# Optimization experiments

Measured on AMD Instinct MI355X. Metric: run time of the kernel, lower is better.

## Reference

```python
import jax, jax.numpy as jnp
import numpy as np
from jax import lax

B, L, P, CIN, N, HD, PH, K = 2048, 96, 96, 8, 64, 64, 8, 3
DIM_C = CIN * N  # 512


def _silu(x):
    return x * jax.nn.sigmoid(x)


def _lin(x, w, b):
    return x @ w.T + b


def setup_inputs() -> dict:
    key = jax.random.key(0)
    ks = iter(jax.random.split(key, 64))

    def w(shape):
        fan_in = shape[-1]
        return (jax.random.normal(next(ks), shape, jnp.float32) / np.sqrt(fan_in)).astype(jnp.float32)

    inp = {"x": jax.random.normal(next(ks), (B, L, CIN), jnp.float32)}
    # x_proj: 5 Linears (enc_in->h, h->h, h->h, h->h, h->N), SiLU between (dropout=eval/identity)
    inp["xp_w0"] = w((HD, CIN)); inp["xp_b0"] = jnp.zeros((HD,), jnp.float32)
    inp["xp_w1"] = w((HD, HD));  inp["xp_b1"] = jnp.zeros((HD,), jnp.float32)
    inp["xp_w2"] = w((HD, HD));  inp["xp_b2"] = jnp.zeros((HD,), jnp.float32)
    inp["xp_w3"] = w((HD, HD));  inp["xp_b3"] = jnp.zeros((HD,), jnp.float32)
    inp["xp_w4"] = w((N, HD));   inp["xp_b4"] = jnp.zeros((N,), jnp.float32)
    # x_proj_: Linear(N,h), SiLU, Linear(h,N)
    inp["xpp_w0"] = w((HD, N)); inp["xpp_b0"] = jnp.zeros((HD,), jnp.float32)
    inp["xpp_w1"] = w((N, HD)); inp["xpp_b1"] = jnp.zeros((N,), jnp.float32)
    # depthwise dilated Conv1d: weight (N, 1, K)
    inp["conv_w"] = w((N, 1, K)); inp["conv_b"] = jnp.zeros((N,), jnp.float32)
    inp["span_A"] = jnp.asarray(0.1, jnp.float32)
    # compress: Linear(N*L, PH)
    inp["comp_w"] = w((PH, N * L)); inp["comp_b"] = jnp.zeros((PH,), jnp.float32)
    # a_ode.net: Linear(PH,h), SiLU, Linear(h,PH), Tanh
    inp["net_w0"] = w((HD, PH)); inp["net_b0"] = jnp.zeros((HD,), jnp.float32)
    inp["net_w1"] = w((PH, HD)); inp["net_b1"] = jnp.zeros((PH,), jnp.float32)
    # lat2out: Linear(PH,8), SiLU, Linear(8,N)
    inp["lo_w0"] = w((8, PH)); inp["lo_b0"] = jnp.zeros((8,), jnp.float32)
    inp["lo_w1"] = w((N, 8));  inp["lo_b1"] = jnp.zeros((N,), jnp.float32)
    # lat2out_c: Linear(PH,8), SiLU, Linear(8, CIN*N)
    inp["lc_w0"] = w((8, PH));     inp["lc_b0"] = jnp.zeros((8,), jnp.float32)
    inp["lc_w1"] = w((DIM_C, 8));  inp["lc_b1"] = jnp.zeros((DIM_C,), jnp.float32)
    # lat2out_z: Linear(N,N), SiLU, Linear(N, CIN)
    inp["lz_w0"] = w((N, N));   inp["lz_b0"] = jnp.zeros((N,), jnp.float32)
    inp["lz_w1"] = w((CIN, N)); inp["lz_b1"] = jnp.zeros((CIN,), jnp.float32)
    return inp


def reference(x, xp_w0, xp_b0, xp_w1, xp_b1, xp_w2, xp_b2, xp_w3, xp_b3, xp_w4, xp_b4,
              xpp_w0, xpp_b0, xpp_w1, xpp_b1, conv_w, conv_b, span_A, comp_w, comp_b,
              net_w0, net_b0, net_w1, net_b1, lo_w0, lo_b0, lo_w1, lo_b1,
              lc_w0, lc_b0, lc_w1, lc_b1, lz_w0, lz_b0, lz_w1, lz_b1):
    Bsz = x.shape[0]

    def x_proj(t):
        h = _silu(_lin(t, xp_w0, xp_b0))
        h = _silu(_lin(h, xp_w1, xp_b1))
        h = _silu(_lin(h, xp_w2, xp_b2))
        h = _silu(_lin(h, xp_w3, xp_b3))
        return _lin(h, xp_w4, xp_b4)

    x_old = x_proj(x[:, :L])                       # (B, L, N)
    hist = x_old.transpose(0, 2, 1)                # (B, N, L)
    pad = (K - 1) * 2                              # 4
    conv = lax.conv_general_dilated(
        hist, conv_w, window_strides=(1,), padding=[(pad, pad)],
        rhs_dilation=(2,), dimension_numbers=("NCH", "OIH", "NCH"),
        feature_group_count=N) + conv_b[None, :, None]
    hist = _silu(conv)[:, :, -L:]                  # (B, N, L)
    hist_f = hist.transpose(0, 2, 1).reshape(Bsz, L * N)
    vector_F = _lin(hist_f, comp_w, comp_b)        # (B, PH)

    a0 = vector_F
    z0 = x_proj(x[:, L - 1])                       # (B, N)

    # Householder matrix H = I - 2 v v^T with v = normalize(x_proj_(z0))
    v = _lin(_silu(_lin(z0, xpp_w0, xpp_b0)), xpp_w1, xpp_b1)
    v = v / (jnp.linalg.norm(v, axis=-1, keepdims=True) + 1e-8)
    Hh = jnp.eye(N, dtype=x.dtype)[None] - 2.0 * v[:, :, None] * v[:, None, :]  # (B,N,N)

    dt = jnp.clip(span_A, 1e-8, 7.0)               # uniform Euler step size
    s0 = jnp.concatenate([a0, z0], axis=-1)        # (B, PH+N)

    def step(s, _):
        a = s[:, :PH]
        z = s[:, PH:]
        da = jnp.tanh(_lin(_silu(_lin(a, net_w0, net_b0)), net_w1, net_b1))  # (B,PH)
        d = _lin(_silu(_lin(a, lo_w0, lo_b0)), lo_w1, lo_b1)                 # (B,N)
        # dz = H^T diag(d) H z   (fused; avoids materializing A_mat)
        Hz = jnp.einsum('bjk,bk->bj', Hh, z)
        dz = jnp.einsum('bj,bji->bi', d * Hz, Hh)
        s_new = s + dt * jnp.concatenate([da, dz], axis=-1)
        return s_new, s_new

    _, sol = lax.scan(step, s0, None, length=P)    # (P, B, PH+N) == sol[1:]

    c_traj = sol[:, :, :PH]                        # (P, B, PH)
    z_traj = sol[:, :, PH:]                        # (P, B, N)

    C = _lin(_silu(_lin(c_traj, lc_w0, lc_b0)), lc_w1, lc_b1)  # (P, B, CIN*N)
    C = C.reshape(P, Bsz, CIN, N)
    y_hat_c = jnp.einsum('pbcn,pbn->pbc', C, z_traj)           # (P, B, CIN)
    added_z = _lin(_silu(_lin(z_traj, lz_w0, lz_b0)), lz_w1, lz_b1)
    x_pred = (y_hat_c + added_z).transpose(1, 0, 2)            # (B, P, CIN)

    x_rec = x[:, :L, :]
    return (x_rec, x_pred)
```

## Files before the change

### kernel.cpp

```cpp
#include <hip/hip_runtime.h>
#include <cstdint>
#include <cstddef>

#define BB 2048
#define LL 96
#define PP 96
#define NN 64
#define HSTRIDE 68

typedef __attribute__((ext_vector_type(8))) short short8;
typedef __attribute__((ext_vector_type(4))) float f32x4;

union U4S8 { uint4 u; short8 s; };

__device__ __forceinline__ float siluf(float x) {
  return x * __builtin_amdgcn_rcpf(1.0f + __expf(-x));
}
__device__ __forceinline__ float tanhf_fast(float x) {
  return 1.0f - 2.0f * __builtin_amdgcn_rcpf(1.0f + __expf(2.0f * x));
}
__device__ __forceinline__ float rlane(float x, int l) {
  return __int_as_float(__builtin_amdgcn_readlane(__float_as_int(x), l));
}

template <int CTRL>
__device__ __forceinline__ float dppadd(float x) {
  int y = __builtin_amdgcn_update_dpp(0, __float_as_int(x), CTRL, 0xF, 0xF, false);
  return x + __int_as_float(y);
}
template <int CTRL>
__device__ __forceinline__ float dppmov(float x) {
  int y = __builtin_amdgcn_update_dpp(0, __float_as_int(x), CTRL, 0xF, 0xF, false);
  return __int_as_float(y);
}

__device__ __forceinline__ float addswap16(float x) {
#if __has_builtin(__builtin_amdgcn_permlane16_swap)
  auto r = __builtin_amdgcn_permlane16_swap(__float_as_uint(x), __float_as_uint(x), false, false);
  return __uint_as_float(r[0]) + __uint_as_float(r[1]);
#else
  return x + __shfl_xor(x, 16, 64);
#endif
}
__device__ __forceinline__ float addswap32(float x) {
#if __has_builtin(__builtin_amdgcn_permlane32_swap)
  auto r = __builtin_amdgcn_permlane32_swap(__float_as_uint(x), __float_as_uint(x), false, false);
  return __uint_as_float(r[0]) + __uint_as_float(r[1]);
#else
  return x + __shfl_xor(x, 32, 64);
#endif
}
__device__ __forceinline__ float movswap32(float x, bool hi) {
#if __has_builtin(__builtin_amdgcn_permlane32_swap)
  auto r = __builtin_amdgcn_permlane32_swap(__float_as_uint(x), __float_as_uint(x), false, false);
  return __uint_as_float(hi ? r[0] : r[1]);
#else
  return __shfl_xor(x, 32, 64);
#endif
}

__device__ __forceinline__ float wave_sum(float x) {
  x = dppadd<0xB1>(x);
  x = dppadd<0x4E>(x);
  x = dppadd<0x141>(x);
  x = dppadd<0x128>(x);
  x = addswap16(x);
  x = addswap32(x);
  return x;
}

__device__ __forceinline__ uint32_t packpair(float f) {
  uint32_t b = __float_as_uint(f);
  uint32_t h = b & 0xFFFF0000u;
  float r = f - __uint_as_float(h);
  return (h >> 16) | (__float_as_uint(r) & 0xFFFF0000u);
}
__device__ __forceinline__ uint32_t rot16(uint32_t x) {
#if __has_builtin(__builtin_amdgcn_alignbit)
  return __builtin_amdgcn_alignbit(x, x, 16);
#else
  return (x >> 16) | (x << 16);
#endif
}
__device__ __forceinline__ uint4 rot16x4(uint4 u) {
  return make_uint4(rot16(u.x), rot16(u.y), rot16(u.z), rot16(u.w));
}
__device__ __forceinline__ short8 as8(uint4 u) { U4S8 c; c.u = u; return c.s; }

__global__ __launch_bounds__(256, 2) void k_xproj(
    const float* __restrict__ x,
    const float* __restrict__ w0, const float* __restrict__ b0,
    const float* __restrict__ w1, const float* __restrict__ b1,
    const float* __restrict__ w2, const float* __restrict__ b2,
    const float* __restrict__ w3, const float* __restrict__ b3,
    const float* __restrict__ w4, const float* __restrict__ b4,
    float* __restrict__ x_old, float* __restrict__ out)
{
  __shared__ uint32_t hbuf[128 * HSTRIDE];
  __shared__ uint32_t wbufA[64 * HSTRIDE];
  __shared__ uint32_t wbufB[64 * HSTRIDE];
  __shared__ float bs[320];

  int tid = threadIdx.x;
  int wave = tid >> 6, lane = tid & 63;
  int quad = lane >> 4, m16 = lane & 15;
  size_t tokBase = (size_t)blockIdx.x * 128;

  {
    size_t e = tokBase * 8 + (size_t)tid * 4;
    *(float4*)(out + e) = *(const float4*)(x + e);
  }
  if (tid < 64) {
    bs[tid]       = b0[tid];
    bs[64 + tid]  = b1[tid];
    bs[128 + tid] = b2[tid];
    bs[192 + tid] = b3[tid];
    bs[256 + tid] = b4[tid];
  }
  #pragma unroll
  for (int i = 0; i < 4; ++i) {
    int e4 = i * 256 + tid;
    int o = e4 >> 4, k = (e4 & 15) << 2;
    float4 wv = ((const float4*)w1)[e4];
    *(uint4*)(wbufA + o * HSTRIDE + k) =
        make_uint4(packpair(wv.x), packpair(wv.y), packpair(wv.z), packpair(wv.w));
  }
  __syncthreads();

  uint4 A0[2];
  #pragma unroll
  for (int mt = 0; mt < 2; ++mt) {
    uint4 t = make_uint4(0, 0, 0, 0);
    if (quad < 2) {
      const float* xp = x + (tokBase + wave * 32 + mt * 16 + m16) * 8 + quad * 4;
      float4 xa = *(const float4*)xp;
      t = make_uint4(packpair(xa.x), packpair(xa.y), packpair(xa.z), packpair(xa.w));
    }
    A0[mt] = t;
  }
  uint4 B0[4];
  #pragma unroll
  for (int nt = 0; nt < 4; ++nt) {
    uint4 t = make_uint4(0, 0, 0, 0);
    if (quad < 2) {
      const float* wp = w0 + (nt * 16 + m16) * 8 + quad * 4;
      float4 wa = *(const float4*)wp;
      t = make_uint4(packpair(wa.x), packpair(wa.y), packpair(wa.z), packpair(wa.w));
    }
    B0[nt] = t;
  }
  {
    f32x4 acc[2][4];
    #pragma unroll
    for (int mt = 0; mt < 2; ++mt)
      #pragma unroll
      for (int nt = 0; nt < 4; ++nt) {
        float bv = bs[nt * 16 + m16];
        acc[mt][nt] = (f32x4){bv, bv, bv, bv};
      }
    #pragma unroll
    for (int mt = 0; mt < 2; ++mt)
      #pragma unroll
      for (int nt = 0; nt < 4; ++nt)
        acc[mt][nt] = __builtin_amdgcn_mfma_f32_16x16x32_bf16(as8(A0[mt]), as8(B0[nt]), acc[mt][nt], 0, 0, 0);
    #pragma unroll
    for (int mt = 0; mt < 2; ++mt) {
      uint4 As = rot16x4(A0[mt]);
      #pragma unroll
      for (int nt = 0; nt < 4; ++nt)
        acc[mt][nt] = __builtin_amdgcn_mfma_f32_16x16x32_bf16(as8(As), as8(B0[nt]), acc[mt][nt], 0, 0, 0);
    }
    #pragma unroll
    for (int mt = 0; mt < 2; ++mt)
      #pragma unroll
      for (int nt = 0; nt < 4; ++nt)
        #pragma unroll
        for (int r = 0; r < 4; ++r) {
          float s = siluf(acc[mt][nt][r]);
          hbuf[(wave * 32 + mt * 16 + quad * 4 + r) * HSTRIDE + nt * 16 + m16] = packpair(s);
        }
  }

  const float* Ws[4] = {w1, w2, w3, w4};
  uint32_t* cur = wbufA;
  uint32_t* nxt = wbufB;
  #pragma unroll 1
  for (int lyr = 0; lyr < 4; ++lyr) {
    float4 wv[4];
    if (lyr < 3) {
      const float* wn = Ws[lyr + 1];
      #pragma unroll
      for (int i = 0; i < 4; ++i) wv[i] = ((const float4*)wn)[i * 256 + tid];
    }
    uint4 Bf[16];
    #pragma unroll
    for (int nt = 0; nt < 4; ++nt)
      #pragma unroll
      for (int c = 0; c < 4; ++c)
        Bf[nt * 4 + c] = *(const uint4*)(cur + (nt * 16 + m16) * HSTRIDE + c * 16 + quad * 4);
    uint4 Af[8];
    #pragma unroll
    for (int mt = 0; mt < 2; ++mt)
      #pragma unroll
      for (int c = 0; c < 4; ++c)
        Af[mt * 4 + c] = *(const uint4*)(hbuf + (wave * 32 + mt * 16 + m16) * HSTRIDE + c * 16 + quad * 4);

    f32x4 acc[2][4];
    #pragma unroll
    for (int mt = 0; mt < 2; ++mt)
      #pragma unroll
      for (int nt = 0; nt < 4; ++nt) {
        float bv = bs[(lyr + 1) * 64 + nt * 16 + m16];
        acc[mt][nt] = (f32x4){bv, bv, bv, bv};
      }
    #pragma unroll
    for (int c = 0; c < 4; ++c)
      #pragma unroll
      for (int mt = 0; mt < 2; ++mt)
        #pragma unroll
        for (int nt = 0; nt < 4; ++nt)
          acc[mt][nt] = __builtin_amdgcn_mfma_f32_16x16x32_bf16(as8(Af[mt * 4 + c]), as8(Bf[nt * 4 + c]), acc[mt][nt], 0, 0, 0);
    #pragma unroll
    for (int c = 0; c < 4; ++c)
      #pragma unroll
      for (int mt = 0; mt < 2; ++mt) {
        uint4 As = rot16x4(Af[mt * 4 + c]);
        #pragma unroll
        for (int nt = 0; nt < 4; ++nt)
          acc[mt][nt] = __builtin_amdgcn_mfma_f32_16x16x32_bf16(as8(As), as8(Bf[nt * 4 + c]), acc[mt][nt], 0, 0, 0);
      }

    if (lyr < 3) {
      #pragma unroll
      for (int i = 0; i < 4; ++i) {
        int e4 = i * 256 + tid;
        int o = e4 >> 4, k = (e4 & 15) << 2;
        *(uint4*)(nxt + o * HSTRIDE + k) =
            make_uint4(packpair(wv[i].x), packpair(wv[i].y), packpair(wv[i].z), packpair(wv[i].w));
      }
    }

    if (lyr < 3) {
      #pragma unroll
      for (int mt = 0; mt < 2; ++mt)
        #pragma unroll
        for (int nt = 0; nt < 4; ++nt)
          #pragma unroll
          for (int r = 0; r < 4; ++r) {
            float s = siluf(acc[mt][nt][r]);
            hbuf[(wave * 32 + mt * 16 + quad * 4 + r) * HSTRIDE + nt * 16 + m16] = packpair(s);
          }
    } else {
      #pragma unroll
      for (int mt = 0; mt < 2; ++mt)
        #pragma unroll
        for (int nt = 0; nt < 4; ++nt)
          #pragma unroll
          for (int r = 0; r < 4; ++r) {
            size_t t = tokBase + wave * 32 + mt * 16 + quad * 4 + r;
            x_old[t * 64 + nt * 16 + m16] = acc[mt][nt][r];
          }
    }
    __syncthreads();
    uint32_t* tmp = cur; cur = nxt; nxt = tmp;
  }
}

__global__ __launch_bounds__(256) void k_hist(
    const float* __restrict__ x_old,
    const float* __restrict__ conv_w, const float* __restrict__ conv_b,
    const float* __restrict__ comp_w, const float* __restrict__ comp_b,
    const float* __restrict__ xw0, const float* __restrict__ xb0,
    const float* __restrict__ xw1, const float* __restrict__ xb1,
    float* __restrict__ a0_o, float* __restrict__ v_o, float* __restrict__ z0_o)
{
  __shared__ float xo[LL * NN];
  __shared__ float red[32];
  __shared__ float hbuf[64];
  int b = blockIdx.x, tid = threadIdx.x;
  const float* src = x_old + (size_t)b * (LL * NN);
  #pragma unroll
  for (int i = 0; i < 6; ++i) {
    int e = (i * 256 + tid) * 4;
    *(float4*)(xo + e) = *(const float4*)(src + e);
  }
  __syncthreads();
  int c = tid & 63;
  float cw0 = conv_w[c * 3], cw1 = conv_w[c * 3 + 1], cw2 = conv_w[c * 3 + 2];
  float cb = conv_b[c];
  float acc[8];
  #pragma unroll
  for (int q = 0; q < 8; ++q) acc[q] = 0.f;
  #pragma unroll 1
  for (int j = 0; j < 24; ++j) {
    int e = j * 256 + tid;
    int t = e >> 6;
    float s = xo[t * 64 + c] * cw0 + cb;
    if (t + 2 < LL) s += xo[(t + 2) * 64 + c] * cw1;
    if (t + 4 < LL) s += xo[(t + 4) * 64 + c] * cw2;
    float hv = siluf(s);
    #pragma unroll
    for (int q = 0; q < 8; ++q) acc[q] += hv * comp_w[q * 6144 + e];
  }
  #pragma unroll
  for (int q = 0; q < 8; ++q) acc[q] = dppadd<0xB1>(acc[q]);
  #pragma unroll
  for (int q = 0; q < 8; ++q) acc[q] = dppadd<0x4E>(acc[q]);
  #pragma unroll
  for (int q = 0; q < 8; ++q) acc[q] = dppadd<0x141>(acc[q]);
  #pragma unroll
  for (int q = 0; q < 8; ++q) acc[q] = dppadd<0x128>(acc[q]);
  #pragma unroll
  for (int q = 0; q < 8; ++q) acc[q] = addswap16(acc[q]);
  #pragma unroll
  for (int q = 0; q < 8; ++q) acc[q] = addswap32(acc[q]);
  int wave = tid >> 6, lane = tid & 63;
  if (lane < 8) {
    float sel = acc[0];
    #pragma unroll
    for (int q = 1; q < 8; ++q) sel = (lane == q) ? acc[q] : sel;
    red[wave * 8 + lane] = sel;
  }
  __syncthreads();
  if (tid < 8)
    a0_o[b * 8 + tid] = red[tid] + red[8 + tid] + red[16 + tid] + red[24 + tid] + comp_b[tid];
  if (tid < 64) {
    float a2 = xb0[tid];
    #pragma unroll 8
    for (int k = 0; k < 64; ++k) a2 += xw0[tid * 64 + k] * xo[6080 + k];
    hbuf[tid] = siluf(a2);
  }
  __syncthreads();
  float vr = 0.f;
  if (tid < 64) {
    vr = xb1[tid];
    #pragma unroll 8
    for (int k = 0; k < 64; ++k) vr += xw1[tid * 64 + k] * hbuf[k];
  }
  float s2 = wave_sum(vr * vr);
  if (tid < 64) {
    float nrm = sqrtf(s2) + 1e-8f;
    v_o[b * 64 + tid] = vr / nrm;
    z0_o[b * 64 + tid] = xo[6080 + tid];
  }
}

__global__ __launch_bounds__(256) void k_scan(
    const float* __restrict__ a0_i, const float* __restrict__ v_i, const float* __restrict__ z0_i,
    const float* __restrict__ nw0, const float* __restrict__ nb0_p,
    const float* __restrict__ nw1, const float* __restrict__ nb1_p,
    const float* __restrict__ lw0, const float* __restrict__ lb0_p,
    const float* __restrict__ lw1, const float* __restrict__ lb1_p,
    const float* __restrict__ spanA, float* __restrict__ atraj, uint32_t* __restrict__ ztraj)
{
  int tid = threadIdx.x;
  int lane = tid & 63;
  int wv = tid >> 6;
  int b = blockIdx.x * 4 + wv;
  float dt = fminf(fmaxf(spanA[0], 1e-8f), 7.0f);
  int i8 = lane & 7;
  bool hi32 = lane >= 32;
  int rrow = ((lane ^ (lane >> 1)) & 1) | (((lane ^ (lane >> 2)) & 1) << 1) | (((lane >> 5) & 1) << 2);

  float w0r[8], wxl[4], wxp[4], g0r[8], d1r[8];
  #pragma unroll
  for (int i = 0; i < 8; ++i) w0r[i] = nw0[lane * 8 + i];
  #pragma unroll
  for (int j = 0; j < 4; ++j) wxl[j] = nw1[rrow * 64 + (lane ^ j)];
  #pragma unroll
  for (int j = 0; j < 4; ++j) wxp[j] = nw1[(rrow ^ 4) * 64 + (lane ^ j)];
  #pragma unroll
  for (int i = 0; i < 8; ++i) g0r[i] = lw0[i8 * 8 + i];
  #pragma unroll
  for (int i = 0; i < 8; ++i) d1r[i] = lw1[lane * 8 + i];
  float nb0 = nb0_p[lane];
  float nb1r = nb1_p[rrow];
  float lb0o = lb0_p[i8];
  float lb1 = lb1_p[lane];
  float v = v_i[b * 64 + lane];
  float z = z0_i[b * 64 + lane];
  float a_own = a0_i[b * 8 + rrow];
  float t0 = wave_sum(v * z);
  float w = z - 2.0f * t0 * v;
  float a_s[8];
  a_s[0] = rlane(a_own, 0);  a_s[1] = rlane(a_own, 2);
  a_s[2] = rlane(a_own, 4);  a_s[3] = rlane(a_own, 6);
  a_s[4] = rlane(a_own, 32); a_s[5] = rlane(a_own, 34);
  a_s[6] = rlane(a_own, 36); a_s[7] = rlane(a_own, 38);

  float* ab = atraj + (size_t)b * (PP * 8);
  uint32_t* zb = ztraj + (size_t)b * (PP * NN);
  bool astore = (lane & 0x19) == 0;

  auto step_rec = [&]() {
    float u0 = w0r[0] * a_s[0] + w0r[1] * a_s[1];
    float u1 = w0r[2] * a_s[2] + w0r[3] * a_s[3];
    float u2 = w0r[4] * a_s[4] + w0r[5] * a_s[5];
    float u3 = w0r[6] * a_s[6] + w0r[7] * a_s[7];
    float h = siluf(nb0 + ((u0 + u1) + (u2 + u3)));
    float hv1 = dppmov<0xB1>(h);
    float hv2 = dppmov<0x4E>(h);
    float hv3 = dppmov<0x1B>(h);
    float slo = (wxl[0] * h + wxl[1] * hv1) + (wxl[2] * hv2 + wxl[3] * hv3);
    float pre = (wxp[0] * h + wxp[1] * hv1) + (wxp[2] * hv2 + wxp[3] * hv3);
    float ps = slo + movswap32(pre, hi32);
    ps = dppadd<0x141>(ps);
    ps = dppadd<0x128>(ps);
    ps = addswap16(ps);
    float da = tanhf_fast(ps + nb1r);
    float e0 = g0r[0] * a_s[0] + g0r[1] * a_s[1];
    float e1 = g0r[2] * a_s[2] + g0r[3] * a_s[3];
    float e2 = g0r[4] * a_s[4] + g0r[5] * a_s[5];
    float e3 = g0r[6] * a_s[6] + g0r[7] * a_s[7];
    float g_own = siluf(lb0o + ((e0 + e1) + (e2 + e3)));
    float f0 = d1r[0] * rlane(g_own, 0) + d1r[1] * rlane(g_own, 1);
    float f1 = d1r[2] * rlane(g_own, 2) + d1r[3] * rlane(g_own, 3);
    float f2 = d1r[4] * rlane(g_own, 4) + d1r[5] * rlane(g_own, 5);
    float f3 = d1r[6] * rlane(g_own, 6) + d1r[7] * rlane(g_own, 7);
    float d = lb1 + ((f0 + f1) + (f2 + f3));
    a_own += dt * da;
    a_s[0] = rlane(a_own, 0);  a_s[1] = rlane(a_own, 2);
    a_s[2] = rlane(a_own, 4);  a_s[3] = rlane(a_own, 6);
    a_s[4] = rlane(a_own, 32); a_s[5] = rlane(a_own, 34);
    a_s[6] = rlane(a_own, 36); a_s[7] = rlane(a_own, 38);
    w *= (1.0f + dt * d);
  };

  step_rec();
  float wo = w, ao = a_own;
  #pragma unroll 1
  for (int p = 1; p < PP; ++p) {
    float woc = wo, aoc = ao;
    step_rec();
    wo = w; ao = a_own;
    float t1 = wave_sum(v * woc);
    float zv = woc - 2.0f * t1 * v;
    if (astore) ab[(p - 1) * 8 + rrow] = aoc;
    zb[(p - 1) * 64 + lane] = packpair(zv);
  }
  {
    float t1 = wave_sum(v * wo);
    float zv = wo - 2.0f * t1 * v;
    if (astore) ab[(PP - 1) * 8 + rrow] = ao;
    zb[(PP - 1) * 64 + lane] = packpair(zv);
  }
}

__global__ __launch_bounds__(256, 4) void k_post(
    const float* __restrict__ atraj, const uint32_t* __restrict__ ztraj,
    const float* __restrict__ cw0, const float* __restrict__ cb0,
    const float* __restrict__ cw1, const float* __restrict__ cb1,
    const float* __restrict__ zw0, const float* __restrict__ zb0,
    const float* __restrict__ zw1, const float* __restrict__ zb1,
    float* __restrict__ out)
{
  __shared__ uint32_t wbuf[144 * HSTRIDE];
  __shared__ float    cw0s[64];
  __shared__ float    cb0s[8];
  __shared__ float    zb0s[64];
  __shared__ float    zb1s[8];

  int tid = threadIdx.x;
  int wave = tid >> 6, lane = tid & 63;
  int quad = lane >> 4, m16 = lane & 15;
  size_t tokBase = (size_t)blockIdx.x * 64;

  #pragma unroll
  for (int i = 0; i < 36; ++i) {
    int e = i * 256 + tid;
    int o = e >> 6, k = e & 63;
    float wv;
    if (o < 64)       wv = cw1[(((o >> 3) * 64 + k) << 3) + (o & 7)];
    else if (o < 72)  wv = cb1[(o - 64) * 64 + k];
    else if (o < 136) wv = zw0[(o - 72) * 64 + k];
    else              wv = zw1[(o - 136) * 64 + k];
    wbuf[o * HSTRIDE + k] = packpair(wv);
  }
  if (tid < 64) cw0s[tid] = cw0[tid];
  if (tid < 8)  cb0s[tid] = cb0[tid];
  if (tid < 64) zb0s[tid] = zb0[tid];
  if (tid < 8)  zb1s[tid] = zb1[tid];
  __syncthreads();

  const uint32_t* zp = ztraj + (tokBase + wave * 16 + m16) * 64;
  uint4 Az[4], Azr[4];
  #pragma unroll
  for (int c = 0; c < 4; ++c) {
    Az[c]  = *(const uint4*)(zp + c * 16 + quad * 4);
    Azr[c] = rot16x4(Az[c]);
  }

  f32x4 acc1[5];
  #pragma unroll
  for (int nt = 0; nt < 5; ++nt) {
    f32x4 acc = (f32x4){0.f, 0.f, 0.f, 0.f};
    #pragma unroll
    for (int c = 0; c < 4; ++c) {
      uint4 Bf = *(const uint4*)(wbuf + (nt * 16 + m16) * HSTRIDE + c * 16 + quad * 4);
      acc = __builtin_amdgcn_mfma_f32_16x16x32_bf16(as8(Az[c]),  as8(Bf), acc, 0, 0, 0);
      acc = __builtin_amdgcn_mfma_f32_16x16x32_bf16(as8(Azr[c]), as8(Bf), acc, 0, 0, 0);
    }
    acc1[nt] = acc;
  }
  __syncthreads();

  uint32_t* ebuf = wbuf;
  #pragma unroll
  for (int nt = 0; nt < 4; ++nt) {
    f32x4 acc = (f32x4){0.f, 0.f, 0.f, 0.f};
    #pragma unroll
    for (int c = 0; c < 4; ++c) {
      uint4 Bf = *(const uint4*)(wbuf + (72 + nt * 16 + m16) * HSTRIDE + c * 16 + quad * 4);
      acc = __builtin_amdgcn_mfma_f32_16x16x32_bf16(as8(Az[c]),  as8(Bf), acc, 0, 0, 0);
      acc = __builtin_amdgcn_mfma_f32_16x16x32_bf16(as8(Azr[c]), as8(Bf), acc, 0, 0, 0);
    }
    int m = nt * 16 + m16;
    float zbv = zb0s[m];
    #pragma unroll
    for (int r = 0; r < 4; ++r) {
      float e = siluf(acc[r] + zbv);
      ebuf[(wave * 16 + quad * 4 + r) * HSTRIDE + m] = packpair(e);
    }
  }

  f32x4 acc3;
  {
    f32x4 acc = (f32x4){0.f, 0.f, 0.f, 0.f};
    int brow = 136 + (m16 & 7);
    #pragma unroll
    for (int c = 0; c < 4; ++c) {
      uint4 Ez = *(const uint4*)(ebuf + (wave * 16 + m16) * HSTRIDE + c * 16 + quad * 4);
      uint4 Bf = *(const uint4*)(wbuf + brow * HSTRIDE + c * 16 + quad * 4);
      acc = __builtin_amdgcn_mfma_f32_16x16x32_bf16(as8(Ez),         as8(Bf), acc, 0, 0, 0);
      acc = __builtin_amdgcn_mfma_f32_16x16x32_bf16(as8(rot16x4(Ez)), as8(Bf), acc, 0, 0, 0);
    }
    acc3 = acc;
  }

  int j = m16 & 7;
  float cwj[8];
  #pragma unroll
  for (int i = 0; i < 8; ++i) cwj[i] = cw0s[j * 8 + i];
  float cbj = cb0s[j];
  #pragma unroll
  for (int r = 0; r < 4; ++r) {
    size_t idx = tokBase + wave * 16 + quad * 4 + r;
    const float* ap = atraj + idx * 8;
    float4 a0v = *(const float4*)ap;
    float4 a1v = *(const float4*)(ap + 4);
    float g2v = cbj
      + cwj[0] * a0v.x + cwj[1] * a0v.y + cwj[2] * a0v.z + cwj[3] * a0v.w
      + cwj[4] * a1v.x + cwj[5] * a1v.y + cwj[6] * a1v.z + cwj[7] * a1v.w;
    g2v = siluf(g2v);
    float yc[4], qo[4];
    #pragma unroll
    for (int nt = 0; nt < 4; ++nt) {
      float p = acc1[nt][r] * g2v;
      p = dppadd<0xB1>(p);
      p = dppadd<0x4E>(p);
      p = dppadd<0x141>(p);
      yc[nt] = p;
      qo[nt] = dppmov<0x128>(p);
    }
    if (m16 < 8) {
      int cc = m16;
      int nt = cc >> 1;
      float ye = (nt == 0) ? yc[0] : (nt == 1) ? yc[1] : (nt == 2) ? yc[2] : yc[3];
      float yo = (nt == 0) ? qo[0] : (nt == 1) ? qo[1] : (nt == 2) ? qo[2] : qo[3];
      float y = (cc & 1) ? yo : ye;
      y += acc1[4][r] + acc3[r] + zb1s[cc];
      out[(size_t)(BB * LL * 8) + idx * 8 + cc] = y;
    }
  }
}

extern "C" void kernel_launch(void* const* d_in, const int* in_sizes, int n_in,
                              void* d_out, int out_size, void* d_ws, size_t ws_size,
                              hipStream_t stream) {
  const float* x      = (const float*)d_in[0];
  const float* xp_w0  = (const float*)d_in[1];
  const float* xp_b0  = (const float*)d_in[2];
  const float* xp_w1  = (const float*)d_in[3];
  const float* xp_b1  = (const float*)d_in[4];
  const float* xp_w2  = (const float*)d_in[5];
  const float* xp_b2  = (const float*)d_in[6];
  const float* xp_w3  = (const float*)d_in[7];
  const float* xp_b3  = (const float*)d_in[8];
  const float* xp_w4  = (const float*)d_in[9];
  const float* xp_b4  = (const float*)d_in[10];
  const float* xpp_w0 = (const float*)d_in[11];
  const float* xpp_b0 = (const float*)d_in[12];
  const float* xpp_w1 = (const float*)d_in[13];
  const float* xpp_b1 = (const float*)d_in[14];
  const float* conv_w = (const float*)d_in[15];
  const float* conv_b = (const float*)d_in[16];
  const float* span_A = (const float*)d_in[17];
  const float* comp_w = (const float*)d_in[18];
  const float* comp_b = (const float*)d_in[19];
  const float* net_w0 = (const float*)d_in[20];
  const float* net_b0 = (const float*)d_in[21];
  const float* net_w1 = (const float*)d_in[22];
  const float* net_b1 = (const float*)d_in[23];
  const float* lo_w0  = (const float*)d_in[24];
  const float* lo_b0  = (const float*)d_in[25];
  const float* lo_w1  = (const float*)d_in[26];
  const float* lo_b1  = (const float*)d_in[27];
  const float* lc_w0  = (const float*)d_in[28];
  const float* lc_b0  = (const float*)d_in[29];
  const float* lc_w1  = (const float*)d_in[30];
  const float* lc_b1  = (const float*)d_in[31];
  const float* lz_w0  = (const float*)d_in[32];
  const float* lz_b0  = (const float*)d_in[33];
  const float* lz_w1  = (const float*)d_in[34];
  const float* lz_b1  = (const float*)d_in[35];

  float*    ws    = (float*)d_ws;
  float*    x_old = ws;
  uint32_t* ztraj = (uint32_t*)ws;
  float*    atraj = ws + 12582912;
  float*    a0    = ws + 14155776;
  float*    vv    = a0 + 2048 * 8;
  float*    z0    = vv + 2048 * 64;
  float*    out   = (float*)d_out;

  hipLaunchKernelGGL(k_xproj, dim3(1536), dim3(256), 0, stream,
                     x, xp_w0, xp_b0, xp_w1, xp_b1, xp_w2, xp_b2, xp_w3, xp_b3,
                     xp_w4, xp_b4, x_old, out);
  hipLaunchKernelGGL(k_hist, dim3(2048), dim3(256), 0, stream,
                     x_old, conv_w, conv_b, comp_w, comp_b,
                     xpp_w0, xpp_b0, xpp_w1, xpp_b1, a0, vv, z0);
  hipLaunchKernelGGL(k_scan, dim3(512), dim3(256), 0, stream,
                     a0, vv, z0, net_w0, net_b0, net_w1, net_b1,
                     lo_w0, lo_b0, lo_w1, lo_b1, span_A, atraj, ztraj);
  hipLaunchKernelGGL(k_post, dim3(3072), dim3(256), 0, stream,
                     atraj, ztraj, lc_w0, lc_b0, lc_w1, lc_b1,
                     lz_w0, lz_b0, lz_w1, lz_b1, out);
}
```

Before: 296.3 us.

## Make k_post persistent over four tiles with prefetched z fragments

k_post now processes four 64-token tiles per block (768 blocks instead of 3072). It loads the static weights once per block and reloads only the cw1 rows, because ebuf aliases that region. The next tile's z fragment is prefetched during the current tile's compute, and the atraj loads are batched ahead of use. This amortizes weight staging and hides global load latency, at the cost of fewer blocks, less parallelism, and extra syncs per tile.

```diff
diff --git a/kernel.cpp b/kernel.cpp
--- a/kernel.cpp
+++ b/kernel.cpp
@@ -446,6 +446,7 @@
   }
 }
 
+#define TPOST 4
 __global__ __launch_bounds__(256, 4) void k_post(
     const float* __restrict__ atraj, const uint32_t* __restrict__ ztraj,
     const float* __restrict__ cw0, const float* __restrict__ cb0,
@@ -463,15 +464,13 @@
   int tid = threadIdx.x;
   int wave = tid >> 6, lane = tid & 63;
   int quad = lane >> 4, m16 = lane & 15;
-  size_t tokBase = (size_t)blockIdx.x * 64;
-
-  #pragma unroll
-  for (int i = 0; i < 36; ++i) {
+
+  #pragma unroll
+  for (int i = 0; i < 20; ++i) {
     int e = i * 256 + tid;
-    int o = e >> 6, k = e & 63;
+    int o = 64 + (e >> 6), k = e & 63;
     float wv;
-    if (o < 64)       wv = cw1[(((o >> 3) * 64 + k) << 3) + (o & 7)];
-    else if (o < 72)  wv = cb1[(o - 64) * 64 + k];
+    if (o < 72)       wv = cb1[(o - 64) * 64 + k];
     else if (o < 136) wv = zw0[(o - 72) * 64 + k];
     else              wv = zw1[(o - 136) * 64 + k];
     wbuf[o * HSTRIDE + k] = packpair(wv);
@@ -482,94 +481,127 @@
   if (tid < 8)  zb1s[tid] = zb1[tid];
   __syncthreads();
 
-  const uint32_t* zp = ztraj + (tokBase + wave * 16 + m16) * 64;
-  uint4 Az[4], Azr[4];
-  #pragma unroll
-  for (int c = 0; c < 4; ++c) {
-    Az[c]  = *(const uint4*)(zp + c * 16 + quad * 4);
-    Azr[c] = rot16x4(Az[c]);
-  }
-
-  f32x4 acc1[5];
-  #pragma unroll
-  for (int nt = 0; nt < 5; ++nt) {
-    f32x4 acc = (f32x4){0.f, 0.f, 0.f, 0.f};
-    #pragma unroll
-    for (int c = 0; c < 4; ++c) {
-      uint4 Bf = *(const uint4*)(wbuf + (nt * 16 + m16) * HSTRIDE + c * 16 + quad * 4);
-      acc = __builtin_amdgcn_mfma_f32_16x16x32_bf16(as8(Az[c]),  as8(Bf), acc, 0, 0, 0);
-      acc = __builtin_amdgcn_mfma_f32_16x16x32_bf16(as8(Azr[c]), as8(Bf), acc, 0, 0, 0);
-    }
-    acc1[nt] = acc;
-  }
-  __syncthreads();
-
-  uint32_t* ebuf = wbuf;
-  #pragma unroll
-  for (int nt = 0; nt < 4; ++nt) {
-    f32x4 acc = (f32x4){0.f, 0.f, 0.f, 0.f};
-    #pragma unroll
-    for (int c = 0; c < 4; ++c) {
-      uint4 Bf = *(const uint4*)(wbuf + (72 + nt * 16 + m16) * HSTRIDE + c * 16 + quad * 4);
-      acc = __builtin_amdgcn_mfma_f32_16x16x32_bf16(as8(Az[c]),  as8(Bf), acc, 0, 0, 0);
-      acc = __builtin_amdgcn_mfma_f32_16x16x32_bf16(as8(Azr[c]), as8(Bf), acc, 0, 0, 0);
-    }
-    int m = nt * 16 + m16;
-    float zbv = zb0s[m];
-    #pragma unroll
-    for (int r = 0; r < 4; ++r) {
-      float e = siluf(acc[r] + zbv);
-      ebuf[(wave * 16 + quad * 4 + r) * HSTRIDE + m] = packpair(e);
-    }
-  }
-
-  f32x4 acc3;
-  {
-    f32x4 acc = (f32x4){0.f, 0.f, 0.f, 0.f};
-    int brow = 136 + (m16 & 7);
-    #pragma unroll
-    for (int c = 0; c < 4; ++c) {
-      uint4 Ez = *(const uint4*)(ebuf + (wave * 16 + m16) * HSTRIDE + c * 16 + quad * 4);
-      uint4 Bf = *(const uint4*)(wbuf + brow * HSTRIDE + c * 16 + quad * 4);
-      acc = __builtin_amdgcn_mfma_f32_16x16x32_bf16(as8(Ez),         as8(Bf), acc, 0, 0, 0);
-      acc = __builtin_amdgcn_mfma_f32_16x16x32_bf16(as8(rot16x4(Ez)), as8(Bf), acc, 0, 0, 0);
-    }
-    acc3 = acc;
-  }
-
   int j = m16 & 7;
   float cwj[8];
   #pragma unroll
   for (int i = 0; i < 8; ++i) cwj[i] = cw0s[j * 8 + i];
   float cbj = cb0s[j];
-  #pragma unroll
-  for (int r = 0; r < 4; ++r) {
-    size_t idx = tokBase + wave * 16 + quad * 4 + r;
-    const float* ap = atraj + idx * 8;
-    float4 a0v = *(const float4*)ap;
-    float4 a1v = *(const float4*)(ap + 4);
-    float g2v = cbj
-      + cwj[0] * a0v.x + cwj[1] * a0v.y + cwj[2] * a0v.z + cwj[3] * a0v.w
-      + cwj[4] * a1v.x + cwj[5] * a1v.y + cwj[6] * a1v.z + cwj[7] * a1v.w;
-    g2v = siluf(g2v);
-    float yc[4], qo[4];
+
+  uint32_t* ebuf = wbuf;
+
+  uint4 Azn[4];
+  {
+    const uint32_t* zp = ztraj + ((size_t)(blockIdx.x * TPOST) * 64 + wave * 16 + m16) * 64;
+    #pragma unroll
+    for (int c = 0; c < 4; ++c) Azn[c] = *(const uint4*)(zp + c * 16 + quad * 4);
+  }
+
+  #pragma unroll 1
+  for (int tt = 0; tt < TPOST; ++tt) {
+    size_t tokBase = (size_t)(blockIdx.x * TPOST + tt) * 64;
+
+    __syncthreads();
+    #pragma unroll
+    for (int i = 0; i < 16; ++i) {
+      int e = i * 256 + tid;
+      int o = e >> 6, k = e & 63;
+      wbuf[o * HSTRIDE + k] = packpair(cw1[(((o >> 3) * 64 + k) << 3) + (o & 7)]);
+    }
+    __syncthreads();
+
+    uint4 Az[4], Azr[4];
+    #pragma unroll
+    for (int c = 0; c < 4; ++c) { Az[c] = Azn[c]; Azr[c] = rot16x4(Az[c]); }
+
+    f32x4 acc1[5];
+    #pragma unroll
+    for (int nt = 0; nt < 5; ++nt) {
+      f32x4 acc = (f32x4){0.f, 0.f, 0.f, 0.f};
+      #pragma unroll
+      for (int c = 0; c < 4; ++c) {
+        uint4 Bf = *(const uint4*)(wbuf + (nt * 16 + m16) * HSTRIDE + c * 16 + quad * 4);
+        acc = __builtin_amdgcn_mfma_f32_16x16x32_bf16(as8(Az[c]),  as8(Bf), acc, 0, 0, 0);
+        acc = __builtin_amdgcn_mfma_f32_16x16x32_bf16(as8(Azr[c]), as8(Bf), acc, 0, 0, 0);
+      }
+      acc1[nt] = acc;
+    }
+    __syncthreads();
+
     #pragma unroll
     for (int nt = 0; nt < 4; ++nt) {
-      float p = acc1[nt][r] * g2v;
-      p = dppadd<0xB1>(p);
-      p = dppadd<0x4E>(p);
-      p = dppadd<0x141>(p);
-      yc[nt] = p;
-      qo[nt] = dppmov<0x128>(p);
-    }
-    if (m16 < 8) {
-      int cc = m16;
-      int nt = cc >> 1;
-      float ye = (nt == 0) ? yc[0] : (nt == 1) ? yc[1] : (nt == 2) ? yc[2] : yc[3];
-      float yo = (nt == 0) ? qo[0] : (nt == 1) ? qo[1] : (nt == 2) ? qo[2] : qo[3];
-      float y = (cc & 1) ? yo : ye;
-      y += acc1[4][r] + acc3[r] + zb1s[cc];
-      out[(size_t)(BB * LL * 8) + idx * 8 + cc] = y;
+      f32x4 acc = (f32x4){0.f, 0.f, 0.f, 0.f};
+      #pragma unroll
+      for (int c = 0; c < 4; ++c) {
+        uint4 Bf = *(const uint4*)(wbuf + (72 + nt * 16 + m16) * HSTRIDE + c * 16 + quad * 4);
+        acc = __builtin_amdgcn_mfma_f32_16x16x32_bf16(as8(Az[c]),  as8(Bf), acc, 0, 0, 0);
+        acc = __builtin_amdgcn_mfma_f32_16x16x32_bf16(as8(Azr[c]), as8(Bf), acc, 0, 0, 0);
+      }
+      int m = nt * 16 + m16;
+      float zbv = zb0s[m];
+      #pragma unroll
+      for (int r = 0; r < 4; ++r) {
+        float e = siluf(acc[r] + zbv);
+        ebuf[(wave * 16 + quad * 4 + r) * HSTRIDE + m] = packpair(e);
+      }
+    }
+
+    if (tt + 1 < TPOST) {
+      const uint32_t* zp = ztraj + ((size_t)(blockIdx.x * TPOST + tt + 1) * 64 + wave * 16 + m16) * 64;
+      #pragma unroll
+      for (int c = 0; c < 4; ++c) Azn[c] = *(const uint4*)(zp + c * 16 + quad * 4);
+    }
+
+    f32x4 acc3;
+    {
+      f32x4 acc = (f32x4){0.f, 0.f, 0.f, 0.f};
+      int brow = 136 + (m16 & 7);
+      #pragma unroll
+      for (int c = 0; c < 4; ++c) {
+        uint4 Ez = *(const uint4*)(ebuf + (wave * 16 + m16) * HSTRIDE + c * 16 + quad * 4);
+        uint4 Bf = *(const uint4*)(wbuf + brow * HSTRIDE + c * 16 + quad * 4);
+        acc = __builtin_amdgcn_mfma_f32_16x16x32_bf16(as8(Ez),          as8(Bf), acc, 0, 0, 0);
+        acc = __builtin_amdgcn_mfma_f32_16x16x32_bf16(as8(rot16x4(Ez)), as8(Bf), acc, 0, 0, 0);
+      }
+      acc3 = acc;
+    }
+
+    float4 av[8];
+    {
+      const float* ap0 = atraj + (tokBase + wave * 16 + quad * 4) * 8;
+      #pragma unroll
+      for (int r = 0; r < 4; ++r) {
+        av[2 * r]     = *(const float4*)(ap0 + r * 8);
+        av[2 * r + 1] = *(const float4*)(ap0 + r * 8 + 4);
+      }
+    }
+    #pragma unroll
+    for (int r = 0; r < 4; ++r) {
+      size_t idx = tokBase + wave * 16 + quad * 4 + r;
+      float4 a0v = av[2 * r];
+      float4 a1v = av[2 * r + 1];
+      float g2v = cbj
+        + cwj[0] * a0v.x + cwj[1] * a0v.y + cwj[2] * a0v.z + cwj[3] * a0v.w
+        + cwj[4] * a1v.x + cwj[5] * a1v.y + cwj[6] * a1v.z + cwj[7] * a1v.w;
+      g2v = siluf(g2v);
+      float yc[4], qo[4];
+      #pragma unroll
+      for (int nt = 0; nt < 4; ++nt) {
+        float p = acc1[nt][r] * g2v;
+        p = dppadd<0xB1>(p);
+        p = dppadd<0x4E>(p);
+        p = dppadd<0x141>(p);
+        yc[nt] = p;
+        qo[nt] = dppmov<0x128>(p);
+      }
+      if (m16 < 8) {
+        int cc = m16;
+        int nt = cc >> 1;
+        float ye = (nt == 0) ? yc[0] : (nt == 1) ? yc[1] : (nt == 2) ? yc[2] : yc[3];
+        float yo = (nt == 0) ? qo[0] : (nt == 1) ? qo[1] : (nt == 2) ? qo[2] : qo[3];
+        float y = (cc & 1) ? yo : ye;
+        y += acc1[4][r] + acc3[r] + zb1s[cc];
+        out[(size_t)(BB * LL * 8) + idx * 8 + cc] = y;
+      }
     }
   }
 }
@@ -632,7 +664,7 @@
   hipLaunchKernelGGL(k_scan, dim3(512), dim3(256), 0, stream,
                      a0, vv, z0, net_w0, net_b0, net_w1, net_b1,
                      lo_w0, lo_b0, lo_w1, lo_b1, span_A, atraj, ztraj);
-  hipLaunchKernelGGL(k_post, dim3(3072), dim3(256), 0, stream,
+  hipLaunchKernelGGL(k_post, dim3(768), dim3(256), 0, stream,
                      atraj, ztraj, lc_w0, lc_b0, lc_w1, lc_b1,
                      lz_w0, lz_b0, lz_w1, lz_b1, out);
 }
```

Result: slower. 306.6 us (+3.5%).
